# Kernel optimization log

Hardware: AMD Instinct MI355X
Metric: run time of the kernel (lower is better)

The kernel has to match this reference:

```python
import jax, jax.numpy as jnp
import numpy as np

N, E, C = 50000, 600000, 128
BN_EPS = 1e-5
NORM_EPS = 1e-12


def _edgeconv(x, src, dst, wa, ba, g, be, rm, rv, wb, bb):
    # PyG EdgeConv: message = MLP(concat(x_i, x_j - x_i)); aggr='add' at target i
    x_i = x[dst]                      # [E, C] target features
    x_j = x[src]                      # [E, C] source features
    m = jnp.concatenate([x_i, x_j - x_i], axis=-1)   # [E, 2C]
    m = jax.nn.relu(m @ wa.T + ba)                   # Linear(2C->C) + ReLU
    m = (m - rm) * (g * jax.lax.rsqrt(rv + BN_EPS)) + be  # BatchNorm1d (eval)
    m = m @ wb.T + bb                                # Linear(C->C)
    return jax.ops.segment_sum(m, dst, num_segments=x.shape[0])  # [N, C]


def _lin(k, fan_in, shape):
    bound = 1.0 / np.sqrt(fan_in)
    return jax.random.uniform(k, shape, jnp.float32, -bound, bound)


def setup_inputs() -> dict:
    key = jax.random.key(0)
    ks = jax.random.split(key, 16)
    inp = {
        "x": jax.random.normal(ks[0], (N, C), jnp.float32),
        "edge_index": jax.random.randint(ks[1], (2, E), 0, N, jnp.int64),
    }
    # layer 1 params
    inp["w1a"] = _lin(ks[2], 2 * C, (C, 2 * C)); inp["b1a"] = _lin(ks[3], 2 * C, (C,))
    inp["g1"] = jnp.ones((C,), jnp.float32) + 0.1 * jax.random.normal(ks[4], (C,))
    inp["be1"] = 0.1 * jax.random.normal(ks[5], (C,))
    inp["rm1"] = 0.1 * jax.random.normal(ks[6], (C,))
    inp["rv1"] = 0.5 + jax.random.uniform(ks[7], (C,))
    inp["w1b"] = _lin(ks[8], C, (C, C)); inp["b1b"] = _lin(ks[9], C, (C,))
    # layer 2 params
    inp["w2a"] = _lin(ks[10], 2 * C, (C, 2 * C)); inp["b2a"] = _lin(ks[11], 2 * C, (C,))
    inp["g2"] = jnp.ones((C,), jnp.float32) + 0.1 * jax.random.normal(ks[12], (C,))
    inp["be2"] = 0.1 * jax.random.normal(ks[13], (C,))
    inp["rm2"] = 0.1 * jax.random.normal(ks[14], (C,))
    inp["rv2"] = 0.5 + jax.random.uniform(ks[15], (C,))
    k2 = jax.random.split(ks[15], 2)
    inp["w2b"] = _lin(k2[0], C, (C, C)); inp["b2b"] = _lin(k2[1], C, (C,))
    return inp


def reference(x, edge_index, w1a, b1a, g1, be1, rm1, rv1, w1b, b1b,
              w2a, b2a, g2, be2, rm2, rv2, w2b, b2b):
    src, dst = edge_index[0], edge_index[1]
    # layer 1 (all but last): conv -> relu -> L2 normalize -> dropout(eval=identity)
    h = _edgeconv(x, src, dst, w1a, b1a, g1, be1, rm1, rv1, w1b, b1b)
    h = jax.nn.relu(h)
    h = h / jnp.maximum(jnp.linalg.norm(h, axis=-1, keepdims=True), NORM_EPS)
    # last layer: conv only
    return _edgeconv(h, src, dst, w2a, b2a, g2, be2, rm2, rv2, w2b, b2b)
```

## Files before the change

kernel.cpp:

```cpp
#include <hip/hip_runtime.h>

#define CCH 128
#define WPAD 136
typedef unsigned short ushort;
typedef __attribute__((ext_vector_type(8))) short bf16x8_t;
typedef __attribute__((ext_vector_type(4))) float f32x4;

union ABu { bf16x8_t v; ushort u[8]; uint4 q; };

__device__ __forceinline__ ushort f2b(float f) {
  union { float f; unsigned u; } v{f};
  unsigned r = v.u + 0x7fffu + ((v.u >> 16) & 1u);
  return (ushort)(r >> 16);
}
__device__ __forceinline__ float b2f(ushort s) {
  union { unsigned u; float f; } v{(unsigned)s << 16};
  return v.f;
}

__device__ __forceinline__ int ldidx(const void* ei, size_t i, bool i64) {
  return i64 ? (int)((const long long*)ei)[i] : ((const int*)ei)[i];
}

__global__ void k_init(const unsigned int* __restrict__ eiw, int* __restrict__ flags,
                       int* __restrict__ degcnt, int n2,
                       const float* __restrict__ w1a, const float* __restrict__ w1b,
                       const float* __restrict__ w2a, const float* __restrict__ w2b,
                       ushort* __restrict__ Wcat1, ushort* __restrict__ Wb1,
                       ushort* __restrict__ Wcat2, ushort* __restrict__ Wb2) {
  int b = blockIdx.x, t = threadIdx.x;
  int gid = b * 256 + t;
  if (gid < n2) degcnt[gid] = 0;

  if (b < 128) {
    int i = gid;
    int c = i >> 7, k = i & 127;
    float v = (c < 128) ? w1a[c * 256 + k] - w1a[c * 256 + 128 + k]
                        : w1a[(c - 128) * 256 + 128 + k];
    Wcat1[i] = f2b(v);
    if (i < 16384) Wb1[i] = f2b(w1b[i]);
  } else if (b < 256) {
    int i = gid - 32768;
    int c = i >> 7, k = i & 127;
    float v = (c < 128) ? w2a[c * 256 + k] - w2a[c * 256 + 128 + k]
                        : w2a[(c - 128) * 256 + 128 + k];
    Wcat2[i] = f2b(v);
    if (i < 16384) Wb2[i] = f2b(w2b[i]);
  } else if (b == 256) {
    __shared__ int cz;
    if (t == 0) cz = 0;
    __syncthreads();
    if (eiw[2 * t + 1] != 0u) atomicAdd(&cz, 1);
    __syncthreads();
    if (t == 0) flags[1] = (cz == 0) ? 1 : 0;
  }
}

__global__ void k_hist(const void* __restrict__ ei, int* __restrict__ deg, int E,
                       const int* __restrict__ flags) {
  bool i64 = flags[1] != 0;
  int e = blockIdx.x * 256 + threadIdx.x;
  if (e < E) atomicAdd(&deg[ldidx(ei, (size_t)E + e, i64)], 1);
}

__global__ void k_scan1(const int* __restrict__ deg, int* __restrict__ bsum, int n) {
  __shared__ int s[256];
  int t = threadIdx.x, i = blockIdx.x * 256 + t;
  s[t] = (i < n) ? deg[i] : 0;
  __syncthreads();
  for (int off = 128; off > 0; off >>= 1) {
    if (t < off) s[t] += s[t + off];
    __syncthreads();
  }
  if (t == 0) bsum[blockIdx.x] = s[0];
}

__global__ void k_scan2(const int* __restrict__ bsum, int* __restrict__ boff, int nb) {
  __shared__ int s[256];
  int t = threadIdx.x;
  int v = (t < nb) ? bsum[t] : 0;
  s[t] = v; __syncthreads();
  for (int off = 1; off < 256; off <<= 1) {
    int tv = (t >= off) ? s[t - off] : 0;
    __syncthreads();
    s[t] += tv;
    __syncthreads();
  }
  if (t < nb) boff[t] = s[t] - v;
}

__global__ void k_scan3(const int* __restrict__ deg, const int* __restrict__ boff,
                        int* __restrict__ rowptr, int n, int Etot) {
  __shared__ int s[256];
  int t = threadIdx.x, i = blockIdx.x * 256 + t;
  int v = (i < n) ? deg[i] : 0;
  s[t] = v; __syncthreads();
  for (int off = 1; off < 256; off <<= 1) {
    int tv = (t >= off) ? s[t - off] : 0;
    __syncthreads();
    s[t] += tv;
    __syncthreads();
  }
  if (i < n) rowptr[i] = boff[blockIdx.x] + s[t] - v;
  if (i == 0) rowptr[n] = Etot;
}

__global__ void k_scatter(const void* __restrict__ ei, const int* __restrict__ rowptr,
                          int* __restrict__ cnt, int* __restrict__ esrc, int E,
                          const int* __restrict__ flags) {
  bool i64 = flags[1] != 0;
  int e = blockIdx.x * 256 + threadIdx.x;
  if (e < E) {
    int d = ldidx(ei, (size_t)E + e, i64);
    int s = ldidx(ei, (size_t)e, i64);
    int pos = rowptr[d] + atomicAdd(&cnt[d], 1);
    esrc[pos] = s;
  }
}

template <int EPI, typename TIN>
__global__ __launch_bounds__(256) void k_gemm(const TIN* __restrict__ X,
                                              const ushort* __restrict__ W,
                                              const float* __restrict__ bias,
                                              const int* __restrict__ deg,
                                              void* __restrict__ Y1,
                                              ushort* __restrict__ Y2, int nN) {
  __shared__ ushort wlds[128 * WPAD];
  const int t = threadIdx.x;
  const int wave = t >> 6, lane = t & 63;
  const int ln = lane & 15, quad = lane >> 4;
  const int half = (EPI == 0) ? blockIdx.y : 0;

  const ushort* Wp = W + (size_t)half * 128 * CCH;
  for (int i = t; i < 128 * 16; i += 256) {
    int row = i >> 4, ch = i & 15;
    *(uint4*)&wlds[row * WPAD + ch * 8] = *(const uint4*)&Wp[row * CCH + ch * 8];
  }
  __syncthreads();

  const int rowb = blockIdx.x * 64 + wave * 16;
  const int arow = rowb + ln;

  ABu a[4];
#pragma unroll
  for (int kk = 0; kk < 4; ++kk) {
    if constexpr (sizeof(TIN) == 4) {
      if (arow < nN) {
        const float* xp = (const float*)X + (size_t)arow * CCH + kk * 32 + quad * 8;
        float4 f0 = *(const float4*)xp;
        float4 f1 = *(const float4*)(xp + 4);
        a[kk].u[0] = f2b(f0.x); a[kk].u[1] = f2b(f0.y); a[kk].u[2] = f2b(f0.z); a[kk].u[3] = f2b(f0.w);
        a[kk].u[4] = f2b(f1.x); a[kk].u[5] = f2b(f1.y); a[kk].u[6] = f2b(f1.z); a[kk].u[7] = f2b(f1.w);
      } else a[kk].q = make_uint4(0, 0, 0, 0);
    } else {
      a[kk].q = (arow < nN) ? *(const uint4*)((const ushort*)X + (size_t)arow * CCH + kk * 32 + quad * 8)
                            : make_uint4(0, 0, 0, 0);
    }
  }

  f32x4 acc[8];
#pragma unroll
  for (int s = 0; s < 8; ++s) acc[s] = (f32x4){0.f, 0.f, 0.f, 0.f};

#pragma unroll
  for (int s = 0; s < 8; ++s) {
#pragma unroll
    for (int kk = 0; kk < 4; ++kk) {
      ABu b;
      b.q = *(const uint4*)&wlds[(s * 16 + ln) * WPAD + kk * 32 + quad * 8];
      acc[s] = __builtin_amdgcn_mfma_f32_16x16x32_bf16(a[kk].v, b.v, acc[s], 0, 0, 0);
    }
  }

  if constexpr (EPI == 0) {
    ushort* dst = half ? Y2 : (ushort*)Y1;
#pragma unroll
    for (int s = 0; s < 8; ++s) {
      int col = s * 16 + ln;
      float bv = half ? 0.f : bias[col];
#pragma unroll
      for (int r = 0; r < 4; ++r) {
        int row = rowb + quad * 4 + r;
        if (row < nN) dst[(size_t)row * CCH + col] = f2b(acc[s][r] + bv);
      }
    }
  } else if constexpr (EPI == 1) {
    ushort* H = (ushort*)Y1;
    float biasv[8];
#pragma unroll
    for (int s = 0; s < 8; ++s) biasv[s] = bias[s * 16 + ln];
#pragma unroll
    for (int r = 0; r < 4; ++r) {
      int row = rowb + quad * 4 + r;
      float dn = (row < nN) ? (float)deg[row] : 0.f;
      float vals[8];
      float ss = 0.f;
#pragma unroll
      for (int s = 0; s < 8; ++s) {
        float v = fmaxf(acc[s][r] + dn * biasv[s], 0.f);
        vals[s] = v;
        ss += v * v;
      }
      ss += __shfl_xor(ss, 1, 64);
      ss += __shfl_xor(ss, 2, 64);
      ss += __shfl_xor(ss, 4, 64);
      ss += __shfl_xor(ss, 8, 64);
      float inv = 1.0f / fmaxf(sqrtf(ss), 1e-12f);
      if (row < nN) {
#pragma unroll
        for (int s = 0; s < 8; ++s)
          H[(size_t)row * CCH + s * 16 + ln] = f2b(vals[s] * inv);
      }
    }
  } else {
    float* OUT = (float*)Y1;
    float biasv[8];
#pragma unroll
    for (int s = 0; s < 8; ++s) biasv[s] = bias[s * 16 + ln];
#pragma unroll
    for (int r = 0; r < 4; ++r) {
      int row = rowb + quad * 4 + r;
      if (row >= nN) continue;
      float dn = (float)deg[row];
#pragma unroll
      for (int s = 0; s < 8; ++s)
        OUT[(size_t)row * CCH + s * 16 + ln] = acc[s][r] + dn * biasv[s];
    }
  }
}

__global__ __launch_bounds__(256) void k_aggr(const ushort* __restrict__ A1,
                                              const ushort* __restrict__ A2,
                                              const int* __restrict__ rowptr,
                                              const int* __restrict__ esrc,
                                              const float* __restrict__ g,
                                              const float* __restrict__ be,
                                              const float* __restrict__ rm,
                                              const float* __restrict__ rv,
                                              ushort* __restrict__ M, int nNodes) {
  int node = blockIdx.x * 4 + (threadIdx.x >> 6);
  if (node >= nNodes) return;
  int lane = threadIdx.x & 63;
  int q = lane >> 4;
  int c = (lane & 15) * 8;

  uint4 aq = *(const uint4*)&A1[(size_t)node * CCH + c];
  float a[8] = {b2f((ushort)aq.x), b2f((ushort)(aq.x >> 16)),
                b2f((ushort)aq.y), b2f((ushort)(aq.y >> 16)),
                b2f((ushort)aq.z), b2f((ushort)(aq.z >> 16)),
                b2f((ushort)aq.w), b2f((ushort)(aq.w >> 16))};
  int r0 = rowptr[node], r1 = rowptr[node + 1];
  float s[8] = {0.f, 0.f, 0.f, 0.f, 0.f, 0.f, 0.f, 0.f};

  int e = r0 + q;
  for (; e + 4 < r1; e += 8) {
    int sA = esrc[e], sB = esrc[e + 4];
    uint4 wA = *(const uint4*)&A2[(size_t)sA * CCH + c];
    uint4 wB = *(const uint4*)&A2[(size_t)sB * CCH + c];
    const unsigned* pA = (const unsigned*)&wA;
    const unsigned* pB = (const unsigned*)&wB;
#pragma unroll
    for (int j = 0; j < 4; ++j) {
      s[2*j]   += fmaxf(a[2*j]   + b2f((ushort)pA[j]), 0.f);
      s[2*j+1] += fmaxf(a[2*j+1] + b2f((ushort)(pA[j] >> 16)), 0.f);
      s[2*j]   += fmaxf(a[2*j]   + b2f((ushort)pB[j]), 0.f);
      s[2*j+1] += fmaxf(a[2*j+1] + b2f((ushort)(pB[j] >> 16)), 0.f);
    }
  }
  for (; e < r1; e += 4) {
    int sA = esrc[e];
    uint4 wA = *(const uint4*)&A2[(size_t)sA * CCH + c];
    const unsigned* pA = (const unsigned*)&wA;
#pragma unroll
    for (int j = 0; j < 4; ++j) {
      s[2*j]   += fmaxf(a[2*j]   + b2f((ushort)pA[j]), 0.f);
      s[2*j+1] += fmaxf(a[2*j+1] + b2f((ushort)(pA[j] >> 16)), 0.f);
    }
  }
#pragma unroll
  for (int j = 0; j < 8; ++j) {
    s[j] += __shfl_xor(s[j], 16, 64);
    s[j] += __shfl_xor(s[j], 32, 64);
  }

  if (q == 0) {
    float dn = (float)(r1 - r0);
    unsigned p[4];
#pragma unroll
    for (int j = 0; j < 4; ++j) {
      float sc0 = g[c + 2*j]     * rsqrtf(rv[c + 2*j]     + 1e-5f);
      float sc1 = g[c + 2*j + 1] * rsqrtf(rv[c + 2*j + 1] + 1e-5f);
      float o0 = sc0 * s[2*j]     + dn * (be[c + 2*j]     - rm[c + 2*j]     * sc0);
      float o1 = sc1 * s[2*j + 1] + dn * (be[c + 2*j + 1] - rm[c + 2*j + 1] * sc1);
      p[j] = (unsigned)f2b(o0) | ((unsigned)f2b(o1) << 16);
    }
    *(uint4*)&M[(size_t)node * CCH + c] = make_uint4(p[0], p[1], p[2], p[3]);
  }
}

extern "C" void kernel_launch(void* const* d_in, const int* in_sizes, int n_in,
                              void* d_out, int out_size, void* d_ws, size_t ws_size,
                              hipStream_t stream) {
  const float* x   = (const float*)d_in[0];
  const void*  ei  = d_in[1];
  const float* w1a = (const float*)d_in[2];
  const float* b1a = (const float*)d_in[3];
  const float* g1  = (const float*)d_in[4];
  const float* be1 = (const float*)d_in[5];
  const float* rm1 = (const float*)d_in[6];
  const float* rv1 = (const float*)d_in[7];
  const float* w1b = (const float*)d_in[8];
  const float* b1b = (const float*)d_in[9];
  const float* w2a = (const float*)d_in[10];
  const float* b2a = (const float*)d_in[11];
  const float* g2  = (const float*)d_in[12];
  const float* be2 = (const float*)d_in[13];
  const float* rm2 = (const float*)d_in[14];
  const float* rv2 = (const float*)d_in[15];
  const float* w2b = (const float*)d_in[16];
  const float* b2b = (const float*)d_in[17];

  const int N = in_sizes[0] / CCH;
  const int E = in_sizes[1] / 2;
  const size_t NC = (size_t)N * CCH;

  int* flags  = (int*)d_ws;
  int* deg    = flags + 4;
  int* cnt    = deg + N;
  int* rowptr = cnt + N;
  int* bsum   = rowptr + N + 1;
  int* boff   = bsum + 256;
  int* esrc   = boff + 256;
  uintptr_t pw = ((uintptr_t)(esrc + E) + 63) & ~(uintptr_t)63;
  ushort* Wcat1 = (ushort*)pw;
  ushort* Wcat2 = Wcat1 + 32768;
  ushort* Wb1   = Wcat2 + 32768;
  ushort* Wb2   = Wb1 + 16384;
  uintptr_t pb = ((uintptr_t)(Wb2 + 16384) + 63) & ~(uintptr_t)63;
  ushort* B0 = (ushort*)pb;
  ushort* B1 = B0 + NC;
  ushort* MB = B1 + NC;
  ushort* HB = MB + NC;

  const int gE = (E + 255) / 256;
  const int gS = (N + 255) / 256;
  const int gG = (N + 63) / 64;
  const int gA = (N + 3) / 4;
  int gInit = (2 * N + 255) / 256;
  if (gInit < 257) gInit = 257;

  k_init<<<gInit, 256, 0, stream>>>((const unsigned int*)ei, flags, deg, 2 * N,
                                    w1a, w1b, w2a, w2b, Wcat1, Wb1, Wcat2, Wb2);
  k_hist<<<gE, 256, 0, stream>>>(ei, deg, E, flags);
  k_scan1<<<gS, 256, 0, stream>>>(deg, bsum, N);
  k_scan2<<<1, 256, 0, stream>>>(bsum, boff, gS);
  k_scan3<<<gS, 256, 0, stream>>>(deg, boff, rowptr, N, E);
  k_scatter<<<gE, 256, 0, stream>>>(ei, rowptr, cnt, esrc, E, flags);

  k_gemm<0, float><<<dim3(gG, 2), 256, 0, stream>>>(x, Wcat1, b1a, deg, B0, B1, N);
  k_aggr<<<gA, 256, 0, stream>>>(B0, B1, rowptr, esrc, g1, be1, rm1, rv1, MB, N);
  k_gemm<1, ushort><<<gG, 256, 0, stream>>>(MB, Wb1, b1b, deg, HB, nullptr, N);
  k_gemm<0, ushort><<<dim3(gG, 2), 256, 0, stream>>>(HB, Wcat2, b2a, deg, B0, B1, N);
  k_aggr<<<gA, 256, 0, stream>>>(B0, B1, rowptr, esrc, g2, be2, rm2, rv2, MB, N);
  k_gemm<2, ushort><<<gG, 256, 0, stream>>>(MB, Wb2, b2b, deg, d_out, nullptr, N);
}
```

Before: 300.8 us.

## Fuse preprocessing kernels, double GEMM rows per wave, batch edge index loads in aggregation

Merges weight conversion, x-to-bf16 conversion, index-width detection and degree histogram into one kernel. The first GEMM is fused with the block-sum scan stage, and the three scan kernels are collapsed so each block recomputes its own prefix offset. GEMM waves now process 32 rows with two accumulator sets to reuse B fragments from LDS. Aggregation loads 64 edge indices cooperatively and broadcasts them via shuffles with 4-way unrolled gathers. This cuts launch count and redundant index loads, at the cost of more registers per GEMM wave and per-block recomputation of index width.

```diff
diff --git a/kernel.cpp b/kernel.cpp
--- a/kernel.cpp
+++ b/kernel.cpp
@@ -18,81 +18,73 @@
   return v.f;
 }
 
-__device__ __forceinline__ int ldidx(const void* ei, size_t i, bool i64) {
-  return i64 ? (int)((const long long*)ei)[i] : ((const int*)ei)[i];
-}
-
-__global__ void k_init(const unsigned int* __restrict__ eiw, int* __restrict__ flags,
-                       int* __restrict__ degcnt, int n2,
-                       const float* __restrict__ w1a, const float* __restrict__ w1b,
-                       const float* __restrict__ w2a, const float* __restrict__ w2b,
-                       ushort* __restrict__ Wcat1, ushort* __restrict__ Wb1,
-                       ushort* __restrict__ Wcat2, ushort* __restrict__ Wb2) {
-  int b = blockIdx.x, t = threadIdx.x;
-  int gid = b * 256 + t;
-  if (gid < n2) degcnt[gid] = 0;
-
+__global__ __launch_bounds__(256) void k_pre(const float* __restrict__ x,
+                                             ushort* __restrict__ XB, int nxc,
+                                             const float* __restrict__ w1a,
+                                             const float* __restrict__ w1b,
+                                             const float* __restrict__ w2a,
+                                             const float* __restrict__ w2b,
+                                             ushort* __restrict__ Wcat1, ushort* __restrict__ Wb1,
+                                             ushort* __restrict__ Wcat2, ushort* __restrict__ Wb2,
+                                             const void* __restrict__ ei, int* __restrict__ deg,
+                                             int E, int xcb) {
+  const int b = blockIdx.x, t = threadIdx.x;
   if (b < 128) {
-    int i = gid;
+    int i = b * 256 + t;
     int c = i >> 7, k = i & 127;
     float v = (c < 128) ? w1a[c * 256 + k] - w1a[c * 256 + 128 + k]
                         : w1a[(c - 128) * 256 + 128 + k];
     Wcat1[i] = f2b(v);
     if (i < 16384) Wb1[i] = f2b(w1b[i]);
   } else if (b < 256) {
-    int i = gid - 32768;
+    int i = (b - 128) * 256 + t;
     int c = i >> 7, k = i & 127;
     float v = (c < 128) ? w2a[c * 256 + k] - w2a[c * 256 + 128 + k]
                         : w2a[(c - 128) * 256 + 128 + k];
     Wcat2[i] = f2b(v);
     if (i < 16384) Wb2[i] = f2b(w2b[i]);
-  } else if (b == 256) {
-    __shared__ int cz;
-    if (t == 0) cz = 0;
-    __syncthreads();
-    if (eiw[2 * t + 1] != 0u) atomicAdd(&cz, 1);
-    __syncthreads();
-    if (t == 0) flags[1] = (cz == 0) ? 1 : 0;
-  }
-}
-
-__global__ void k_hist(const void* __restrict__ ei, int* __restrict__ deg, int E,
-                       const int* __restrict__ flags) {
-  bool i64 = flags[1] != 0;
-  int e = blockIdx.x * 256 + threadIdx.x;
-  if (e < E) atomicAdd(&deg[ldidx(ei, (size_t)E + e, i64)], 1);
-}
-
-__global__ void k_scan1(const int* __restrict__ deg, int* __restrict__ bsum, int n) {
+  } else if (b < 256 + xcb) {
+    size_t i = (size_t)(b - 256) * 256 + t;
+    if (i < (size_t)nxc) {
+      const float* xp = x + i * 8;
+      float4 f0 = *(const float4*)xp;
+      float4 f1 = *(const float4*)(xp + 4);
+      ushort o[8] = {f2b(f0.x), f2b(f0.y), f2b(f0.z), f2b(f0.w),
+                     f2b(f1.x), f2b(f1.y), f2b(f1.z), f2b(f1.w)};
+      *(uint4*)&XB[i * 8] = *(const uint4*)o;
+    }
+  } else {
+    __shared__ int nz;
+    if (t == 0) nz = 0;
+    __syncthreads();
+    int e = (b - 256 - xcb) * 256 + t;
+    unsigned hi = (e < E) ? ((const unsigned*)ei)[2 * (size_t)e + 1] : 0u;
+    if (hi) atomicAdd(&nz, 1);
+    __syncthreads();
+    bool i64 = (nz == 0);
+    if (e < E) {
+      int d = i64 ? (int)((const long long*)ei)[(size_t)E + e]
+                  : ((const int*)ei)[(size_t)E + e];
+      atomicAdd(&deg[d], 1);
+    }
+  }
+}
+
+__global__ __launch_bounds__(256) void k_rowptr(const int* __restrict__ deg,
+                                                const int* __restrict__ bsum,
+                                                int* __restrict__ rowptr,
+                                                int n, int nb, int Etot) {
   __shared__ int s[256];
-  int t = threadIdx.x, i = blockIdx.x * 256 + t;
-  s[t] = (i < n) ? deg[i] : 0;
+  const int t = threadIdx.x, b = blockIdx.x;
+  s[t] = (t < nb && t < b) ? bsum[t] : 0;
   __syncthreads();
   for (int off = 128; off > 0; off >>= 1) {
     if (t < off) s[t] += s[t + off];
     __syncthreads();
   }
-  if (t == 0) bsum[blockIdx.x] = s[0];
-}
-
-__global__ void k_scan2(const int* __restrict__ bsum, int* __restrict__ boff, int nb) {
-  __shared__ int s[256];
-  int t = threadIdx.x;
-  int v = (t < nb) ? bsum[t] : 0;
-  s[t] = v; __syncthreads();
-  for (int off = 1; off < 256; off <<= 1) {
-    int tv = (t >= off) ? s[t - off] : 0;
-    __syncthreads();
-    s[t] += tv;
-    __syncthreads();
-  }
-  if (t < nb) boff[t] = s[t] - v;
-}
-
-__global__ void k_scan3(const int* __restrict__ deg, const int* __restrict__ boff,
-                        int* __restrict__ rowptr, int n, int Etot) {
-  __shared__ int s[256];
-  int t = threadIdx.x, i = blockIdx.x * 256 + t;
+  int boffset = s[0];
+  __syncthreads();
+  int i = b * 256 + t;
   int v = (i < n) ? deg[i] : 0;
   s[t] = v; __syncthreads();
   for (int off = 1; off < 256; off <<= 1) {
@@ -101,25 +93,127 @@
     s[t] += tv;
     __syncthreads();
   }
-  if (i < n) rowptr[i] = boff[blockIdx.x] + s[t] - v;
-  if (i == 0) rowptr[n] = Etot;
-}
-
-__global__ void k_scatter(const void* __restrict__ ei, const int* __restrict__ rowptr,
-                          int* __restrict__ cnt, int* __restrict__ esrc, int E,
-                          const int* __restrict__ flags) {
-  bool i64 = flags[1] != 0;
-  int e = blockIdx.x * 256 + threadIdx.x;
+  if (i < n) rowptr[i] = boffset + s[t] - v;
+  if (b == gridDim.x - 1 && t == 0) rowptr[n] = Etot;
+}
+
+__global__ __launch_bounds__(256) void k_scatter(const void* __restrict__ ei,
+                                                 const int* __restrict__ rowptr,
+                                                 int* __restrict__ cnt,
+                                                 int* __restrict__ esrc, int E) {
+  __shared__ int nz;
+  const int t = threadIdx.x;
+  if (t == 0) nz = 0;
+  __syncthreads();
+  int e = blockIdx.x * 256 + t;
+  unsigned hi = (e < E) ? ((const unsigned*)ei)[2 * (size_t)e + 1] : 0u;
+  if (hi) atomicAdd(&nz, 1);
+  __syncthreads();
+  bool i64 = (nz == 0);
   if (e < E) {
-    int d = ldidx(ei, (size_t)E + e, i64);
-    int s = ldidx(ei, (size_t)e, i64);
+    int d, sv;
+    if (i64) {
+      sv = (int)((const long long*)ei)[(size_t)e];
+      d  = (int)((const long long*)ei)[(size_t)E + e];
+    } else {
+      sv = ((const int*)ei)[(size_t)e];
+      d  = ((const int*)ei)[(size_t)E + e];
+    }
     int pos = rowptr[d] + atomicAdd(&cnt[d], 1);
-    esrc[pos] = s;
-  }
-}
-
-template <int EPI, typename TIN>
-__global__ __launch_bounds__(256) void k_gemm(const TIN* __restrict__ X,
+    esrc[pos] = sv;
+  }
+}
+
+__device__ __forceinline__ void gemm_core(const ushort* __restrict__ XB,
+                                          const ushort* __restrict__ wlds,
+                                          int rowb, int ln, int quad, int nN,
+                                          f32x4 acc0[8], f32x4 acc1[8]) {
+  const int ar0 = rowb + ln, ar1 = rowb + 16 + ln;
+  ABu a0[4], a1[4];
+#pragma unroll
+  for (int kk = 0; kk < 4; ++kk) {
+    a0[kk].q = (ar0 < nN) ? *(const uint4*)(XB + (size_t)ar0 * CCH + kk * 32 + quad * 8)
+                          : make_uint4(0, 0, 0, 0);
+    a1[kk].q = (ar1 < nN) ? *(const uint4*)(XB + (size_t)ar1 * CCH + kk * 32 + quad * 8)
+                          : make_uint4(0, 0, 0, 0);
+  }
+#pragma unroll
+  for (int s = 0; s < 8; ++s) {
+    acc0[s] = (f32x4){0.f, 0.f, 0.f, 0.f};
+    acc1[s] = (f32x4){0.f, 0.f, 0.f, 0.f};
+  }
+#pragma unroll
+  for (int s = 0; s < 8; ++s) {
+#pragma unroll
+    for (int kk = 0; kk < 4; ++kk) {
+      ABu b;
+      b.q = *(const uint4*)&wlds[(s * 16 + ln) * WPAD + kk * 32 + quad * 8];
+      acc0[s] = __builtin_amdgcn_mfma_f32_16x16x32_bf16(a0[kk].v, b.v, acc0[s], 0, 0, 0);
+      acc1[s] = __builtin_amdgcn_mfma_f32_16x16x32_bf16(a1[kk].v, b.v, acc1[s], 0, 0, 0);
+    }
+  }
+}
+
+__device__ __forceinline__ void stage_w(const ushort* __restrict__ Wp,
+                                        ushort* __restrict__ wlds, int t) {
+  for (int i = t; i < 128 * 16; i += 256) {
+    int row = i >> 4, ch = i & 15;
+    *(uint4*)&wlds[row * WPAD + ch * 8] = *(const uint4*)&Wp[row * CCH + ch * 8];
+  }
+}
+
+__device__ __forceinline__ void epi0(f32x4 acc[8], int rowb, int ln, int quad, int nN,
+                                     const float* bias, int half, ushort* dst) {
+#pragma unroll
+  for (int s = 0; s < 8; ++s) {
+    int col = s * 16 + ln;
+    float bv = half ? 0.f : bias[col];
+#pragma unroll
+    for (int r = 0; r < 4; ++r) {
+      int row = rowb + quad * 4 + r;
+      if (row < nN) dst[(size_t)row * CCH + col] = f2b(acc[s][r] + bv);
+    }
+  }
+}
+
+__global__ __launch_bounds__(256) void k_mix1(const ushort* __restrict__ XB,
+                                              const ushort* __restrict__ Wcat,
+                                              const float* __restrict__ bias,
+                                              ushort* __restrict__ A1,
+                                              ushort* __restrict__ A2, int nN,
+                                              const int* __restrict__ deg,
+                                              int* __restrict__ bsum, int gH, int n) {
+  __shared__ ushort wlds[128 * WPAD];
+  const int t = threadIdx.x;
+  if ((int)blockIdx.x >= 2 * gH) {
+    int* s = (int*)wlds;
+    int bb = blockIdx.x - 2 * gH;
+    int i = bb * 256 + t;
+    s[t] = (i < n) ? deg[i] : 0;
+    __syncthreads();
+    for (int off = 128; off > 0; off >>= 1) {
+      if (t < off) s[t] += s[t + off];
+      __syncthreads();
+    }
+    if (t == 0) bsum[bb] = s[0];
+    return;
+  }
+  const int half = (int)blockIdx.x >= gH;
+  const int bx = half ? blockIdx.x - gH : blockIdx.x;
+  stage_w(Wcat + (size_t)half * 128 * CCH, wlds, t);
+  __syncthreads();
+  const int wave = t >> 6, lane = t & 63;
+  const int ln = lane & 15, quad = lane >> 4;
+  const int rowb = bx * 128 + wave * 32;
+  f32x4 acc0[8], acc1[8];
+  gemm_core(XB, wlds, rowb, ln, quad, nN, acc0, acc1);
+  ushort* dst = half ? A2 : A1;
+  epi0(acc0, rowb, ln, quad, nN, bias, half, dst);
+  epi0(acc1, rowb + 16, ln, quad, nN, bias, half, dst);
+}
+
+template <int EPI>
+__global__ __launch_bounds__(256) void k_gemm(const ushort* __restrict__ XB,
                                               const ushort* __restrict__ W,
                                               const float* __restrict__ bias,
                                               const int* __restrict__ deg,
@@ -127,105 +221,67 @@
                                               ushort* __restrict__ Y2, int nN) {
   __shared__ ushort wlds[128 * WPAD];
   const int t = threadIdx.x;
+  const int half = (EPI == 0) ? blockIdx.y : 0;
+  stage_w(W + (size_t)half * 128 * CCH, wlds, t);
+  __syncthreads();
   const int wave = t >> 6, lane = t & 63;
   const int ln = lane & 15, quad = lane >> 4;
-  const int half = (EPI == 0) ? blockIdx.y : 0;
-
-  const ushort* Wp = W + (size_t)half * 128 * CCH;
-  for (int i = t; i < 128 * 16; i += 256) {
-    int row = i >> 4, ch = i & 15;
-    *(uint4*)&wlds[row * WPAD + ch * 8] = *(const uint4*)&Wp[row * CCH + ch * 8];
-  }
-  __syncthreads();
-
-  const int rowb = blockIdx.x * 64 + wave * 16;
-  const int arow = rowb + ln;
-
-  ABu a[4];
-#pragma unroll
-  for (int kk = 0; kk < 4; ++kk) {
-    if constexpr (sizeof(TIN) == 4) {
-      if (arow < nN) {
-        const float* xp = (const float*)X + (size_t)arow * CCH + kk * 32 + quad * 8;
-        float4 f0 = *(const float4*)xp;
-        float4 f1 = *(const float4*)(xp + 4);
-        a[kk].u[0] = f2b(f0.x); a[kk].u[1] = f2b(f0.y); a[kk].u[2] = f2b(f0.z); a[kk].u[3] = f2b(f0.w);
-        a[kk].u[4] = f2b(f1.x); a[kk].u[5] = f2b(f1.y); a[kk].u[6] = f2b(f1.z); a[kk].u[7] = f2b(f1.w);
-      } else a[kk].q = make_uint4(0, 0, 0, 0);
-    } else {
-      a[kk].q = (arow < nN) ? *(const uint4*)((const ushort*)X + (size_t)arow * CCH + kk * 32 + quad * 8)
-                            : make_uint4(0, 0, 0, 0);
-    }
-  }
-
-  f32x4 acc[8];
-#pragma unroll
-  for (int s = 0; s < 8; ++s) acc[s] = (f32x4){0.f, 0.f, 0.f, 0.f};
-
-#pragma unroll
-  for (int s = 0; s < 8; ++s) {
-#pragma unroll
-    for (int kk = 0; kk < 4; ++kk) {
-      ABu b;
-      b.q = *(const uint4*)&wlds[(s * 16 + ln) * WPAD + kk * 32 + quad * 8];
-      acc[s] = __builtin_amdgcn_mfma_f32_16x16x32_bf16(a[kk].v, b.v, acc[s], 0, 0, 0);
-    }
-  }
+  const int rowb = blockIdx.x * 128 + wave * 32;
+  f32x4 acc0[8], acc1[8];
+  gemm_core(XB, wlds, rowb, ln, quad, nN, acc0, acc1);
 
   if constexpr (EPI == 0) {
     ushort* dst = half ? Y2 : (ushort*)Y1;
-#pragma unroll
-    for (int s = 0; s < 8; ++s) {
-      int col = s * 16 + ln;
-      float bv = half ? 0.f : bias[col];
-#pragma unroll
-      for (int r = 0; r < 4; ++r) {
-        int row = rowb + quad * 4 + r;
-        if (row < nN) dst[(size_t)row * CCH + col] = f2b(acc[s][r] + bv);
-      }
-    }
+    epi0(acc0, rowb, ln, quad, nN, bias, half, dst);
+    epi0(acc1, rowb + 16, ln, quad, nN, bias, half, dst);
   } else if constexpr (EPI == 1) {
     ushort* H = (ushort*)Y1;
     float biasv[8];
 #pragma unroll
     for (int s = 0; s < 8; ++s) biasv[s] = bias[s * 16 + ln];
-#pragma unroll
-    for (int r = 0; r < 4; ++r) {
-      int row = rowb + quad * 4 + r;
-      float dn = (row < nN) ? (float)deg[row] : 0.f;
-      float vals[8];
-      float ss = 0.f;
-#pragma unroll
-      for (int s = 0; s < 8; ++s) {
-        float v = fmaxf(acc[s][r] + dn * biasv[s], 0.f);
-        vals[s] = v;
-        ss += v * v;
+    auto epi = [&](f32x4* acc, int rb) {
+#pragma unroll
+      for (int r = 0; r < 4; ++r) {
+        int row = rb + quad * 4 + r;
+        float dn = (row < nN) ? (float)deg[row] : 0.f;
+        float vals[8];
+        float ss = 0.f;
+#pragma unroll
+        for (int s = 0; s < 8; ++s) {
+          float v = fmaxf(acc[s][r] + dn * biasv[s], 0.f);
+          vals[s] = v;
+          ss += v * v;
+        }
+        ss += __shfl_xor(ss, 1, 64);
+        ss += __shfl_xor(ss, 2, 64);
+        ss += __shfl_xor(ss, 4, 64);
+        ss += __shfl_xor(ss, 8, 64);
+        float inv = 1.0f / fmaxf(sqrtf(ss), 1e-12f);
+        if (row < nN) {
+#pragma unroll
+          for (int s = 0; s < 8; ++s)
+            H[(size_t)row * CCH + s * 16 + ln] = f2b(vals[s] * inv);
+        }
       }
-      ss += __shfl_xor(ss, 1, 64);
-      ss += __shfl_xor(ss, 2, 64);
-      ss += __shfl_xor(ss, 4, 64);
-      ss += __shfl_xor(ss, 8, 64);
-      float inv = 1.0f / fmaxf(sqrtf(ss), 1e-12f);
-      if (row < nN) {
-#pragma unroll
-        for (int s = 0; s < 8; ++s)
-          H[(size_t)row * CCH + s * 16 + ln] = f2b(vals[s] * inv);
-      }
-    }
+    };
+    epi(acc0, rowb); epi(acc1, rowb + 16);
   } else {
     float* OUT = (float*)Y1;
     float biasv[8];
 #pragma unroll
     for (int s = 0; s < 8; ++s) biasv[s] = bias[s * 16 + ln];
-#pragma unroll
-    for (int r = 0; r < 4; ++r) {
-      int row = rowb + quad * 4 + r;
-      if (row >= nN) continue;
-      float dn = (float)deg[row];
-#pragma unroll
-      for (int s = 0; s < 8; ++s)
-        OUT[(size_t)row * CCH + s * 16 + ln] = acc[s][r] + dn * biasv[s];
-    }
+    auto epi = [&](f32x4* acc, int rb) {
+#pragma unroll
+      for (int r = 0; r < 4; ++r) {
+        int row = rb + quad * 4 + r;
+        if (row >= nN) continue;
+        float dn = (float)deg[row];
+#pragma unroll
+        for (int s = 0; s < 8; ++s)
+          OUT[(size_t)row * CCH + s * 16 + ln] = acc[s][r] + dn * biasv[s];
+      }
+    };
+    epi(acc0, rowb); epi(acc1, rowb + 16);
   }
 }
 
@@ -252,30 +308,39 @@
   int r0 = rowptr[node], r1 = rowptr[node + 1];
   float s[8] = {0.f, 0.f, 0.f, 0.f, 0.f, 0.f, 0.f, 0.f};
 
-  int e = r0 + q;
-  for (; e + 4 < r1; e += 8) {
-    int sA = esrc[e], sB = esrc[e + 4];
-    uint4 wA = *(const uint4*)&A2[(size_t)sA * CCH + c];
-    uint4 wB = *(const uint4*)&A2[(size_t)sB * CCH + c];
-    const unsigned* pA = (const unsigned*)&wA;
-    const unsigned* pB = (const unsigned*)&wB;
+  auto acc8 = [&](uint4 w) {
+    const unsigned* p = (const unsigned*)&w;
 #pragma unroll
     for (int j = 0; j < 4; ++j) {
-      s[2*j]   += fmaxf(a[2*j]   + b2f((ushort)pA[j]), 0.f);
-      s[2*j+1] += fmaxf(a[2*j+1] + b2f((ushort)(pA[j] >> 16)), 0.f);
-      s[2*j]   += fmaxf(a[2*j]   + b2f((ushort)pB[j]), 0.f);
-      s[2*j+1] += fmaxf(a[2*j+1] + b2f((ushort)(pB[j] >> 16)), 0.f);
-    }
-  }
-  for (; e < r1; e += 4) {
-    int sA = esrc[e];
-    uint4 wA = *(const uint4*)&A2[(size_t)sA * CCH + c];
-    const unsigned* pA = (const unsigned*)&wA;
-#pragma unroll
-    for (int j = 0; j < 4; ++j) {
-      s[2*j]   += fmaxf(a[2*j]   + b2f((ushort)pA[j]), 0.f);
-      s[2*j+1] += fmaxf(a[2*j+1] + b2f((ushort)(pA[j] >> 16)), 0.f);
-    }
+      s[2*j]   += fmaxf(a[2*j]   + b2f((ushort)p[j]), 0.f);
+      s[2*j+1] += fmaxf(a[2*j+1] + b2f((ushort)(p[j] >> 16)), 0.f);
+    }
+  };
+
+  for (int base = r0; base < r1; base += 64) {
+    int navail = r1 - base; if (navail > 64) navail = 64;
+    int myi = (lane < navail) ? esrc[base + lane] : 0;
+    int g4 = navail >> 2, tail = navail & 3;
+    int j = 0;
+    for (; j + 4 <= g4; j += 4) {
+      int p0 = j * 4 + q;
+      int i0 = __shfl(myi, p0, 64);
+      int i1 = __shfl(myi, p0 + 4, 64);
+      int i2 = __shfl(myi, p0 + 8, 64);
+      int i3 = __shfl(myi, p0 + 12, 64);
+      uint4 w0 = *(const uint4*)&A2[(size_t)i0 * CCH + c];
+      uint4 w1 = *(const uint4*)&A2[(size_t)i1 * CCH + c];
+      uint4 w2 = *(const uint4*)&A2[(size_t)i2 * CCH + c];
+      uint4 w3 = *(const uint4*)&A2[(size_t)i3 * CCH + c];
+      acc8(w0); acc8(w1); acc8(w2); acc8(w3);
+    }
+    for (; j < g4; ++j) {
+      int i0 = __shfl(myi, j * 4 + q, 64);
+      acc8(*(const uint4*)&A2[(size_t)i0 * CCH + c]);
+    }
+    int pt = g4 * 4 + q; if (pt > 63) pt = 63;
+    int it = __shfl(myi, pt, 64);
+    if (q < tail) acc8(*(const uint4*)&A2[(size_t)it * CCH + c]);
   }
 #pragma unroll
   for (int j = 0; j < 8; ++j) {
@@ -324,43 +389,40 @@
   const int E = in_sizes[1] / 2;
   const size_t NC = (size_t)N * CCH;
 
-  int* flags  = (int*)d_ws;
-  int* deg    = flags + 4;
+  int* deg    = (int*)d_ws;
   int* cnt    = deg + N;
   int* rowptr = cnt + N;
   int* bsum   = rowptr + N + 1;
-  int* boff   = bsum + 256;
-  int* esrc   = boff + 256;
+  int* esrc   = bsum + 256;
   uintptr_t pw = ((uintptr_t)(esrc + E) + 63) & ~(uintptr_t)63;
   ushort* Wcat1 = (ushort*)pw;
   ushort* Wcat2 = Wcat1 + 32768;
   ushort* Wb1   = Wcat2 + 32768;
   ushort* Wb2   = Wb1 + 16384;
   uintptr_t pb = ((uintptr_t)(Wb2 + 16384) + 63) & ~(uintptr_t)63;
-  ushort* B0 = (ushort*)pb;
+  ushort* XB = (ushort*)pb;
+  ushort* B0 = XB + NC;
   ushort* B1 = B0 + NC;
   ushort* MB = B1 + NC;
   ushort* HB = MB + NC;
 
-  const int gE = (E + 255) / 256;
-  const int gS = (N + 255) / 256;
-  const int gG = (N + 63) / 64;
-  const int gA = (N + 3) / 4;
-  int gInit = (2 * N + 255) / 256;
-  if (gInit < 257) gInit = 257;
-
-  k_init<<<gInit, 256, 0, stream>>>((const unsigned int*)ei, flags, deg, 2 * N,
-                                    w1a, w1b, w2a, w2b, Wcat1, Wb1, Wcat2, Wb2);
-  k_hist<<<gE, 256, 0, stream>>>(ei, deg, E, flags);
-  k_scan1<<<gS, 256, 0, stream>>>(deg, bsum, N);
-  k_scan2<<<1, 256, 0, stream>>>(bsum, boff, gS);
-  k_scan3<<<gS, 256, 0, stream>>>(deg, boff, rowptr, N, E);
-  k_scatter<<<gE, 256, 0, stream>>>(ei, rowptr, cnt, esrc, E, flags);
-
-  k_gemm<0, float><<<dim3(gG, 2), 256, 0, stream>>>(x, Wcat1, b1a, deg, B0, B1, N);
+  const int gE  = (E + 255) / 256;
+  const int gS  = (N + 255) / 256;
+  const int gH  = (N + 127) / 128;
+  const int gA  = (N + 3) / 4;
+  const int nxc = (int)(NC / 8);
+  const int xcb = (nxc + 255) / 256;
+
+  hipMemsetAsync(deg, 0, sizeof(int) * 2 * (size_t)N, stream);
+  k_pre<<<256 + xcb + gE, 256, 0, stream>>>(x, XB, nxc, w1a, w1b, w2a, w2b,
+                                            Wcat1, Wb1, Wcat2, Wb2, ei, deg, E, xcb);
+  k_mix1<<<2 * gH + gS, 256, 0, stream>>>(XB, Wcat1, b1a, B0, B1, N, deg, bsum, gH, N);
+  k_rowptr<<<gS, 256, 0, stream>>>(deg, bsum, rowptr, N, gS, E);
+  k_scatter<<<gE, 256, 0, stream>>>(ei, rowptr, cnt, esrc, E);
+
   k_aggr<<<gA, 256, 0, stream>>>(B0, B1, rowptr, esrc, g1, be1, rm1, rv1, MB, N);
-  k_gemm<1, ushort><<<gG, 256, 0, stream>>>(MB, Wb1, b1b, deg, HB, nullptr, N);
-  k_gemm<0, ushort><<<dim3(gG, 2), 256, 0, stream>>>(HB, Wcat2, b2a, deg, B0, B1, N);
+  k_gemm<1><<<gH, 256, 0, stream>>>(MB, Wb1, b1b, deg, HB, nullptr, N);
+  k_gemm<0><<<dim3(gH, 2), 256, 0, stream>>>(HB, Wcat2, b2a, deg, B0, B1, N);
   k_aggr<<<gA, 256, 0, stream>>>(B0, B1, rowptr, esrc, g2, be2, rm2, rv2, MB, N);
-  k_gemm<2, ushort><<<gG, 256, 0, stream>>>(MB, Wb2, b2b, deg, d_out, nullptr, N);
-}
+  k_gemm<2><<<gH, 256, 0, stream>>>(MB, Wb2, b2b, deg, d_out, nullptr, N);
+}
```

After: 299.9 us. Within noise of the previous version (-0.3%).
